# Optimization experiments

Measured on AMD Instinct MI355X. Metric: run time of the kernel, lower is better.

Reference implementation:

```python
import jax, jax.numpy as jnp
import numpy as np

N_NODES = 5000
K_POOL = 30
BN_EPS = 1e-5


def setup_inputs() -> dict:
    key = jax.random.key(0)
    ks = jax.random.split(key, 16)
    B, N, Din, C, H, OUT, E = 32, N_NODES, 16, 64, 128, 2, 80000
    F_tot = Din + 3 * C  # concat of input + 3 conv layers = 208
    return {
        "x": jax.random.normal(ks[0], (B, N, Din), jnp.float32),
        "age": jax.random.uniform(ks[1], (B,), jnp.float32) * 100.0,
        "edge_attr": jax.random.uniform(ks[2], (E,), jnp.float32) + 0.1,
        "W0": jax.random.normal(ks[3], (Din, C), jnp.float32) * 0.1,
        "b0": jnp.zeros((C,), jnp.float32),
        "W1": jax.random.normal(ks[4], (C, C), jnp.float32) * 0.1,
        "b1": jnp.zeros((C,), jnp.float32),
        "W2": jax.random.normal(ks[5], (C, C), jnp.float32) * 0.1,
        "b2": jnp.zeros((C,), jnp.float32),
        "g0": jnp.ones((C,), jnp.float32),
        "be0": jnp.zeros((C,), jnp.float32),
        "g1": jnp.ones((C,), jnp.float32),
        "be1": jnp.zeros((C,), jnp.float32),
        "mW0": jax.random.normal(ks[6], (K_POOL * F_tot + 1, H), jnp.float32) * 0.02,
        "mb0": jnp.zeros((H,), jnp.float32),
        "mW1": jax.random.normal(ks[7], (H, OUT), jnp.float32) * 0.1,
        "mb1": jnp.zeros((OUT,), jnp.float32),
        "edge_row": jax.random.randint(ks[8], (E,), 0, N, jnp.int32),
        "edge_col": jax.random.randint(ks[9], (E,), 0, N, jnp.int32),
    }


def _spmm(xw, rows, cols, nv):
    # xw: (B, N, C); out[b, r] = sum_{edges (r,c)} nv * xw[b, c]
    def one(xb):
        return jax.ops.segment_sum(xb[cols] * nv[:, None], rows, num_segments=N_NODES)
    return jax.vmap(one)(xw)


def reference(x, age, edge_attr, W0, b0, W1, b1, W2, b2, g0, be0, g1, be1,
              mW0, mb0, mW1, mb1, edge_row, edge_col):
    N = N_NODES
    # GCN normalization on A + I (gcn_norm with edge weights, self-loop value 1)
    loop = jnp.arange(N, dtype=edge_row.dtype)
    rows = jnp.concatenate([edge_row, loop])
    cols = jnp.concatenate([edge_col, loop])
    vals = jnp.concatenate([edge_attr, jnp.ones((N,), edge_attr.dtype)])
    deg = jax.ops.segment_sum(vals, rows, num_segments=N)
    dinv = jnp.where(deg > 0, jax.lax.rsqrt(jnp.maximum(deg, 1e-12)), 0.0)
    nv = dinv[rows] * vals * dinv[cols]

    feats = [x]
    h = x
    convs = [(W0, b0), (W1, b1), (W2, b2)]
    bns = [(g0, be0), (g1, be1)]
    for i, (W, b) in enumerate(convs):
        h = _spmm(h @ W, rows, cols, nv) + b  # GCNConv
        if i < len(convs) - 1:
            g, be = bns[i]
            mu = jnp.mean(h, axis=(0, 1))   # BatchNorm1d over flattened (B*N, C)
            var = jnp.var(h, axis=(0, 1))
            h = (h - mu) * jax.lax.rsqrt(var + BN_EPS) * g + be
        h = jax.nn.relu(h)  # dropout p=0.0 -> identity
        feats.append(h)

    z = jnp.concatenate(feats, axis=-1)  # (B, N, 208)
    # global_sort_pool: sort nodes by last feature channel, descending, take top-k
    order = jnp.argsort(-z[:, :, -1], axis=1)[:, :K_POOL]  # (B, k)
    zk = jnp.take_along_axis(z, order[:, :, None], axis=1)  # (B, k, 208)
    flat = zk.reshape(z.shape[0], -1)
    flat = jnp.concatenate([flat, age[:, None]], axis=1)  # append age scalar

    hm = jax.nn.relu(flat @ mW0 + mb0)  # MLP head
    out = hm @ mW1 + mb1
    return jax.nn.log_softmax(out, axis=-1)
```

## Files before the change

### kernel.cpp

```cpp
#include <hip/hip_runtime.h>
#include <math.h>

#define NN    5000
#define NE    80000
#define NB    32
#define DIN   16
#define CH    64
#define KPOOL 30
#define FTOT  208
#define FLATW 6241
#define NH    128
#define NG    8
#define GB    4
#define NPB   16
#define NPAD  5008
#define NEPAD (NE + 4 * NN)
#define NSLOT 32



__global__ void k_init(float* deg, int* counts, float* stats, float* hm, int* perm) {
    int i = blockIdx.x * 256 + threadIdx.x;
    if (i < NN) { deg[i] = 1.0f; counts[i] = 0; }
    if (i < 2 * NSLOT * 128) stats[i] = 0.0f;
    if (i < 4096) hm[i] = 0.0f;
    if (i >= NN && i < NPAD) perm[i] = NN;
}

#define NEB 313
__global__ void k_edgetr(const float* __restrict__ attr, const int* __restrict__ erow,
                         float* deg, int* counts,
                         const float* __restrict__ x, float* __restrict__ xt) {
    if (blockIdx.x < NEB) {
        int e = blockIdx.x * 256 + threadIdx.x;
        if (e < NE) {
            int r = erow[e];
            atomicAdd(&deg[r], attr[e]);
            atomicAdd(&counts[r], 1);
        }
    } else {
        int idx = (blockIdx.x - NEB) * 256 + threadIdx.x;
        if (idx >= NB * NN) return;
        int b = idx / NN, n = idx % NN;
        int g = b >> 2, bi = b & 3;
        const float4* src = (const float4*)(x + (size_t)idx * DIN);
        float4* dst = (float4*)(xt + (((size_t)g * NN + n) * GB + bi) * DIN);
        dst[0] = src[0]; dst[1] = src[1]; dst[2] = src[2]; dst[3] = src[3];
    }
}

__global__ __launch_bounds__(1024) void k_scan(const int* __restrict__ counts,
                                               const float* __restrict__ deg,
                                               int* rowptr, int* cursor, float* dinv,
                                               int* perm) {
    __shared__ int wsum[16], woff[16];
    __shared__ int carry_sh;
    __shared__ int hist[256];
    int t = threadIdx.x;
    int lane = t & 63, wid = t >> 6;
    if (t == 0) carry_sh = 0;
    if (t < 256) hist[t] = 0;
    __syncthreads();
    for (int base = 0; base < NN; base += 1024) {
        int carry = carry_sh;
        int i = base + t;
        int v = 0;
        if (i < NN) {
            v = (counts[i] + 3) & ~3;
            dinv[i] = 1.0f / sqrtf(deg[i]);
            atomicAdd(&hist[255 - min(v >> 2, 255)], 1);
        }
        int s = v;
#pragma unroll
        for (int off = 1; off < 64; off <<= 1) {
            int o = __shfl_up(s, off);
            if (lane >= off) s += o;
        }
        if (lane == 63) wsum[wid] = s;
        __syncthreads();
        if (t < 16) {
            int w = wsum[t];
#pragma unroll
            for (int off = 1; off < 16; off <<= 1) {
                int o = __shfl_up(w, off);
                if (t >= off) w += o;
            }
            woff[t] = w;
        }
        __syncthreads();
        int inc = s + (wid > 0 ? woff[wid - 1] : 0) + carry;
        if (i < NN) {
            rowptr[i + 1] = inc;
            cursor[i] = inc - v;
        }
        if (t == 1023) carry_sh = carry + woff[15];
        __syncthreads();
    }
    if (t == 0) rowptr[0] = 0;
    int mycnt = (t < 256) ? hist[t] : 0;
    for (int off = 1; off < 256; off <<= 1) {
        int v = (t < 256 && t >= off) ? hist[t - off] : 0;
        __syncthreads();
        if (t < 256) hist[t] += v;
        __syncthreads();
    }
    if (t < 256) hist[t] -= mycnt;
    __syncthreads();
    for (int i = t; i < NN; i += 1024) {
        int b = 255 - min(((counts[i] + 3) & ~3) >> 2, 255);
        int pos = atomicAdd(&hist[b], 1);
        perm[pos] = i;
    }
}

__global__ void k_build(const int* __restrict__ erow, const int* __restrict__ ecol,
                        const float* __restrict__ attr, const float* __restrict__ dinv,
                        const int* __restrict__ counts, const int* __restrict__ rowptr,
                        int* cursor, int* csr_col, float* csr_nv) {
    int t = blockIdx.x * 256 + threadIdx.x;
    if (t < NE) {
        int r = erow[t], c = ecol[t];
        int pos = atomicAdd(&cursor[r], 1);
        csr_col[pos] = c;
        csr_nv[pos] = dinv[r] * attr[t] * dinv[c];
    } else if (t - NE < NN) {
        int i = t - NE;
        int cnt = counts[i];
        int pcnt = (cnt + 3) & ~3;
        int base = rowptr[i + 1] - pcnt;
        for (int p = base + cnt; p < base + pcnt; ++p) { csr_col[p] = i; csr_nv[p] = 0.0f; }
    }
}

template<int ACT>
__device__ __forceinline__ float4 actv(float4 v, float4 s, float4 t) {
    if (ACT) {
        v.x = fmaxf(fmaf(v.x, s.x, t.x), 0.f);
        v.y = fmaxf(fmaf(v.y, s.y, t.y), 0.f);
        v.z = fmaxf(fmaf(v.z, s.z, t.z), 0.f);
        v.w = fmaxf(fmaf(v.w, s.w, t.w), 0.f);
    }
    return v;
}
__device__ __forceinline__ void fma4(float4& a, float w, float4 v) {
    a.x = fmaf(w, v.x, a.x); a.y = fmaf(w, v.y, a.y);
    a.z = fmaf(w, v.z, a.z); a.w = fmaf(w, v.w, a.w);
}

template<int CIN, int ACT, int STATS, int SCORE>
__global__ __launch_bounds__(256) void k_layer(
        const float* __restrict__ in, const float* __restrict__ bnstats,
        const float* __restrict__ gamma, const float* __restrict__ beta,
        const float* __restrict__ W, const float* __restrict__ bias,
        const int* __restrict__ rowptr, const int* __restrict__ csr_col,
        const float* __restrict__ csr_nv, const float* __restrict__ dinv,
        const int* __restrict__ perm,
        float* __restrict__ out, float* __restrict__ stats,
        float* __restrict__ score) {
    constexpr int ALS = (CIN == 64) ? 68 : 20;
    __shared__ float As[4 * 16 * ALS];
    __shared__ float stl[ACT ? 128 : 4];
    int tid = threadIdx.x;
    int wid = tid >> 6, lane = tid & 63;
    int g = blockIdx.x & 7;
    int nb = (blockIdx.x >> 3) * NPB;
    int base = nb + wid * 4;
    float* Aw = As + wid * 16 * ALS;
    const int4 pid = *(const int4*)(perm + base);

    if (ACT) {
        if (tid < 64) {
            float su = 0.f, qu = 0.f;
#pragma unroll
            for (int s = 0; s < NSLOT; ++s) {
                su += bnstats[s * 128 + tid];
                qu += bnstats[s * 128 + 64 + tid];
            }
            const float inv = 1.0f / (float)(NB * NN);
            float mu = su * inv;
            float var = qu * inv - mu * mu;
            float sc = gamma[tid] / sqrtf(var + 1e-5f);
            stl[tid] = sc;
            stl[64 + tid] = fmaf(-mu, sc, beta[tid]);
        }
        __syncthreads();
    }

    if (CIN == 64) {
        const float4* __restrict__ in4 = (const float4*)in + (size_t)g * NN * 64;
        int c4 = lane & 15, bi = lane >> 4;
        float4 sv = {1.f,1.f,1.f,1.f}, tv = {0.f,0.f,0.f,0.f};
        if (ACT) { sv = ((const float4*)stl)[c4]; tv = ((const float4*)(stl + 64))[c4]; }
#pragma unroll
        for (int pr = 0; pr < 2; ++pr) {
            int id0 = (pr == 0) ? pid.x : pid.z;
            int id1 = (pr == 0) ? pid.y : pid.w;
            bool vn0 = id0 < NN, vn1 = id1 < NN;
            int rc0 = vn0 ? id0 : 0, rc1 = vn1 ? id1 : 0;
            float dd0 = dinv[rc0]; dd0 *= dd0;
            float dd1 = dinv[rc1]; dd1 *= dd1;
            float4 a0 = {0.f,0.f,0.f,0.f}, a1 = {0.f,0.f,0.f,0.f};
            {
                float4 v0 = actv<ACT>(in4[(size_t)rc0 * 64 + lane], sv, tv);
                float4 v1 = actv<ACT>(in4[(size_t)rc1 * 64 + lane], sv, tv);
                if (vn0) { a0.x = dd0 * v0.x; a0.y = dd0 * v0.y; a0.z = dd0 * v0.z; a0.w = dd0 * v0.w; }
                if (vn1) { a1.x = dd1 * v1.x; a1.y = dd1 * v1.y; a1.z = dd1 * v1.z; a1.w = dd1 * v1.w; }
            }
            int p0a = rowptr[rc0], na = vn0 ? (rowptr[rc0 + 1] - p0a) >> 2 : 0;
            int p0b = rowptr[rc1], nbv = vn1 ? (rowptr[rc1 + 1] - p0b) >> 2 : 0;
            int mx = max(na, nbv);
            for (int bb = 0; bb < mx; ++bb) {
                int ea = min(p0a + 4 * bb, NEPAD - 4);
                int eb = min(p0b + 4 * bb, NEPAD - 4);
                bool va = bb < na, vb = bb < nbv;
                int4   ca = *(const int4*)(csr_col + ea);
                float4 wa = *(const float4*)(csr_nv + ea);
                int4   cb = *(const int4*)(csr_col + eb);
                float4 wb = *(const float4*)(csr_nv + eb);
                if (!va) { wa.x = 0.f; wa.y = 0.f; wa.z = 0.f; wa.w = 0.f;
                           ca.x = 0; ca.y = 0; ca.z = 0; ca.w = 0; }
                if (!vb) { wb.x = 0.f; wb.y = 0.f; wb.z = 0.f; wb.w = 0.f;
                           cb.x = 0; cb.y = 0; cb.z = 0; cb.w = 0; }
                float4 u0 = in4[(size_t)ca.x * 64 + lane];
                float4 u1 = in4[(size_t)ca.y * 64 + lane];
                float4 u2 = in4[(size_t)ca.z * 64 + lane];
                float4 u3 = in4[(size_t)ca.w * 64 + lane];
                float4 t0 = in4[(size_t)cb.x * 64 + lane];
                float4 t1 = in4[(size_t)cb.y * 64 + lane];
                float4 t2 = in4[(size_t)cb.z * 64 + lane];
                float4 t3 = in4[(size_t)cb.w * 64 + lane];
                fma4(a0, wa.x, actv<ACT>(u0, sv, tv));
                fma4(a0, wa.y, actv<ACT>(u1, sv, tv));
                fma4(a0, wa.z, actv<ACT>(u2, sv, tv));
                fma4(a0, wa.w, actv<ACT>(u3, sv, tv));
                fma4(a1, wb.x, actv<ACT>(t0, sv, tv));
                fma4(a1, wb.y, actv<ACT>(t1, sv, tv));
                fma4(a1, wb.z, actv<ACT>(t2, sv, tv));
                fma4(a1, wb.w, actv<ACT>(t3, sv, tv));
            }
            *(float4*)(Aw + ((pr * 2 + 0) * 4 + bi) * ALS + c4 * 4) = a0;
            *(float4*)(Aw + ((pr * 2 + 1) * 4 + bi) * ALS + c4 * 4) = a1;
        }
    } else {
        const float* __restrict__ inr = in + (size_t)g * NN * 64;
        int ids[4] = {pid.x, pid.y, pid.z, pid.w};
#pragma unroll
        for (int i = 0; i < 4; ++i) {
            int r = ids[i];
            float a = 0.f;
            if (r < NN) {
                float d = dinv[r];
                a = d * d * inr[(size_t)r * 64 + lane];
                int p0 = rowptr[r], p1 = rowptr[r + 1];
                for (int e = p0; e < p1; e += 4) {
                    int4   cc = *(const int4*)(csr_col + e);
                    float4 ww = *(const float4*)(csr_nv + e);
                    float v0 = inr[(size_t)cc.x * 64 + lane];
                    float v1 = inr[(size_t)cc.y * 64 + lane];
                    float v2 = inr[(size_t)cc.z * 64 + lane];
                    float v3 = inr[(size_t)cc.w * 64 + lane];
                    a = fmaf(ww.x, v0, a);
                    a = fmaf(ww.y, v1, a);
                    a = fmaf(ww.z, v2, a);
                    a = fmaf(ww.w, v3, a);
                }
            }
            Aw[(i * 4 + (lane >> 4)) * ALS + (lane & 15)] = a;
        }
    }

    int colq = lane & 15, rowq = lane >> 4;
    int node = (rowq == 0) ? pid.x : (rowq == 1) ? pid.y : (rowq == 2) ? pid.z : pid.w;

    if (!SCORE) {
        const float4* __restrict__ W4 = (const float4*)W;
        float4 bb = ((const float4*)bias)[colq];
        float4 o[4];
#pragma unroll
        for (int i = 0; i < 4; ++i) o[i] = bb;
#pragma unroll 8
        for (int k = 0; k < CIN; ++k) {
            float4 w4 = W4[k * 16 + colq];
#pragma unroll
            for (int i = 0; i < 4; ++i) {
                float a = Aw[(rowq * 4 + i) * ALS + k];
                fma4(o[i], a, w4);
            }
        }
        if (node < NN) {
            float4* __restrict__ op = (float4*)(out + ((size_t)g * NN + node) * 256);
#pragma unroll
            for (int i = 0; i < 4; ++i) op[i * 16 + colq] = o[i];
        }

        if (STATS) {
            float4 s4 = {0,0,0,0}, q4 = {0,0,0,0};
            if (node < NN) {
#pragma unroll
                for (int i = 0; i < 4; ++i) {
                    s4.x += o[i].x; s4.y += o[i].y; s4.z += o[i].z; s4.w += o[i].w;
                    q4.x = fmaf(o[i].x, o[i].x, q4.x); q4.y = fmaf(o[i].y, o[i].y, q4.y);
                    q4.z = fmaf(o[i].z, o[i].z, q4.z); q4.w = fmaf(o[i].w, o[i].w, q4.w);
                }
            }
            s4.x += __shfl_xor(s4.x, 16); s4.y += __shfl_xor(s4.y, 16);
            s4.z += __shfl_xor(s4.z, 16); s4.w += __shfl_xor(s4.w, 16);
            q4.x += __shfl_xor(q4.x, 16); q4.y += __shfl_xor(q4.y, 16);
            q4.z += __shfl_xor(q4.z, 16); q4.w += __shfl_xor(q4.w, 16);
            s4.x += __shfl_xor(s4.x, 32); s4.y += __shfl_xor(s4.y, 32);
            s4.z += __shfl_xor(s4.z, 32); s4.w += __shfl_xor(s4.w, 32);
            q4.x += __shfl_xor(q4.x, 32); q4.y += __shfl_xor(q4.y, 32);
            q4.z += __shfl_xor(q4.z, 32); q4.w += __shfl_xor(q4.w, 32);
            __syncthreads();
            if (lane < 16) {
                float* S = As + wid * 128;
                *(float4*)(S + lane * 8) = s4;
                *(float4*)(S + lane * 8 + 4) = q4;
            }
            __syncthreads();
            if (tid < 64) {
                int cq = tid >> 2, comp = tid & 3;
                float s = 0.f, q = 0.f;
#pragma unroll
                for (int w = 0; w < 4; ++w) {
                    s += As[w * 128 + cq * 8 + comp];
                    q += As[w * 128 + cq * 8 + 4 + comp];
                }
                float* sl = stats + (blockIdx.x & (NSLOT - 1)) * 128;
                atomicAdd(&sl[tid], s);
                atomicAdd(&sl[64 + tid], q);
            }
        }
    } else {
        if (node < NN) {
            float4* __restrict__ op = (float4*)(out + ((size_t)g * NN + node) * 256);
#pragma unroll
            for (int i = 0; i < 4; ++i)
                op[i * 16 + colq] = *(const float4*)(Aw + (rowq * 4 + i) * ALS + colq * 4);
        }
        if (lane < 16) {
            int q = lane >> 2;
            int nd = (q == 0) ? pid.x : (q == 1) ? pid.y : (q == 2) ? pid.z : pid.w;
            if (nd < NN) {
                float s = bias[63];
                const float* Ar = Aw + lane * ALS;
#pragma unroll 8
                for (int k = 0; k < 64; ++k)
                    s = fmaf(Ar[k], W[k * 64 + 63], s);
                score[((size_t)g * NN + nd) * 4 + (lane & 3)] = fmaxf(s, 0.f);
            }
        }
    }
}

__global__ void k_bnfin(const float* __restrict__ stats,
                        const float* __restrict__ g0, const float* __restrict__ be0,
                        const float* __restrict__ g1, const float* __restrict__ be1,
                        float* st) {
    int tid = threadIdx.x;
    int c = tid & 63, layer = tid >> 6;
    const float* sb = stats + layer * NSLOT * 128;
    float su = 0.f, qu = 0.f;
#pragma unroll
    for (int s = 0; s < NSLOT; ++s) {
        su += sb[s * 128 + c];
        qu += sb[s * 128 + 64 + c];
    }
    const float inv = 1.0f / (float)(NB * NN);
    float mu = su * inv;
    float var = qu * inv - mu * mu;
    float g = layer ? g1[c] : g0[c];
    float be = layer ? be1[c] : be0[c];
    float sc = g / sqrtf(var + 1e-5f);
    st[layer * 128 + c] = sc;
    st[layer * 128 + 64 + c] = fmaf(-mu, sc, be);
}

__global__ __launch_bounds__(1024) void k_toppool(const float* __restrict__ sc, int* order) {
    __shared__ unsigned long long wbest[16];
    __shared__ unsigned long long winner;
    int b = blockIdx.x, tid = threadIdx.x;
    int g = b >> 2, bi = b & 3;
    int lane = tid & 63, wid = tid >> 6;
    unsigned long long key[5];
#pragma unroll
    for (int j = 0; j < 5; ++j) {
        int n = tid + j * 1024;
        unsigned long long k = 0;
        if (n < NN) {
            float v = sc[((size_t)g * NN + n) * GB + bi];
            k = ((unsigned long long)__float_as_uint(v) << 32) | (unsigned int)(NN - n);
        }
        key[j] = k;
    }
    for (int k = 0; k < KPOOL; ++k) {
        unsigned long long best = key[0];
#pragma unroll
        for (int j = 1; j < 5; ++j) best = (key[j] > best) ? key[j] : best;
#pragma unroll
        for (int off = 1; off < 64; off <<= 1) {
            unsigned long long o = __shfl_xor(best, off);
            best = (o > best) ? o : best;
        }
        if (lane == 0) wbest[wid] = best;
        __syncthreads();
        if (tid == 0) {
            unsigned long long w = wbest[0];
#pragma unroll
            for (int i = 1; i < 16; ++i) w = (wbest[i] > w) ? wbest[i] : w;
            winner = w;
            order[b * KPOOL + k] = NN - (int)(w & 0xFFFFFFFFu);
        }
        __syncthreads();
        int n = NN - (int)(winner & 0xFFFFFFFFu);
        if ((n & 1023) == tid) key[n >> 10] = 0;
    }
}

__global__ void k_gather(const float* __restrict__ xt, const float* __restrict__ h1,
                         const float* __restrict__ h2, const float* __restrict__ agg,
                         const float* __restrict__ W2, const float* __restrict__ b2,
                         const float* __restrict__ st, const float* __restrict__ age,
                         const int* __restrict__ order, float* __restrict__ flat) {
    int bk = blockIdx.x;
    int b = bk / KPOOL, k = bk % KPOOL;
    int n = order[bk];
    int g = b >> 2, bi = b & 3;
    size_t node = (size_t)g * NN + n;
    int f = threadIdx.x;
    float val = 0.f;
    if (f < DIN) {
        val = xt[(node * GB + bi) * DIN + f];
    } else if (f < DIN + CH) {
        int c = f - DIN;
        val = fmaxf(fmaf(h1[(node * GB + bi) * CH + c], st[c], st[64 + c]), 0.f);
    } else if (f < DIN + 2 * CH) {
        int c = f - DIN - CH;
        val = fmaxf(fmaf(h2[(node * GB + bi) * CH + c], st[128 + c], st[192 + c]), 0.f);
    } else if (f < FTOT) {
        int c = f - DIN - 2 * CH;
        const float* __restrict__ Ar = agg + (node * GB + bi) * CH;
        float s = b2[c];
#pragma unroll 8
        for (int kk = 0; kk < 64; ++kk)
            s = fmaf(Ar[kk], W2[kk * 64 + c], s);
        val = fmaxf(s, 0.f);
    }
    if (f < FTOT) flat[(size_t)b * FLATW + k * FTOT + f] = val;
    if (bk == 0 && f >= FTOT && f < FTOT + NB)
        flat[(size_t)(f - FTOT) * FLATW + (FLATW - 1)] = age[f - FTOT];
}

__global__ void k_head1(const float* __restrict__ flat, const float* __restrict__ mW0,
                        float* hm) {
    int tid = threadIdx.x;
    int j4 = (tid & 31) * 4;
    int b0 = (tid >> 5) * 4;
    int kbase = blockIdx.x * 64;
    float acc[4][4];
#pragma unroll
    for (int i = 0; i < 4; i++)
#pragma unroll
        for (int jj = 0; jj < 4; jj++) acc[i][jj] = 0.f;
    int kend = FLATW - kbase; if (kend > 64) kend = 64;
    for (int kk = 0; kk < kend; ++kk) {
        int k = kbase + kk;
        float4 w = *(const float4*)(mW0 + (size_t)k * NH + j4);
#pragma unroll
        for (int i = 0; i < 4; i++) {
            float fv = flat[(size_t)(b0 + i) * FLATW + k];
            acc[i][0] = fmaf(fv, w.x, acc[i][0]);
            acc[i][1] = fmaf(fv, w.y, acc[i][1]);
            acc[i][2] = fmaf(fv, w.z, acc[i][2]);
            acc[i][3] = fmaf(fv, w.w, acc[i][3]);
        }
    }
#pragma unroll
    for (int i = 0; i < 4; i++)
#pragma unroll
        for (int jj = 0; jj < 4; jj++)
            atomicAdd(&hm[(size_t)(b0 + i) * NH + j4 + jj], acc[i][jj]);
}

__global__ void k_head2(const float* __restrict__ hm, const float* __restrict__ mb0,
                        const float* __restrict__ mW1, const float* __restrict__ mb1,
                        float* __restrict__ out) {
    __shared__ float vals[64];
    int tid = threadIdx.x;
    int b = tid >> 1, o = tid & 1;
    float acc = mb1[o];
    for (int j = 0; j < NH; ++j) {
        float hv = fmaxf(hm[b * NH + j] + mb0[j], 0.f);
        acc = fmaf(hv, mW1[j * 2 + o], acc);
    }
    vals[tid] = acc;
    __syncthreads();
    float v0 = vals[b * 2], v1 = vals[b * 2 + 1];
    float m = fmaxf(v0, v1);
    float lse = m + logf(expf(v0 - m) + expf(v1 - m));
    out[tid] = acc - lse;
}

extern "C" void kernel_launch(void* const* d_in, const int* in_sizes, int n_in,
                              void* d_out, int out_size, void* d_ws, size_t ws_size,
                              hipStream_t stream) {
    const float* x    = (const float*)d_in[0];
    const float* age  = (const float*)d_in[1];
    const float* attr = (const float*)d_in[2];
    const float* W0   = (const float*)d_in[3];
    const float* b0   = (const float*)d_in[4];
    const float* W1   = (const float*)d_in[5];
    const float* b1   = (const float*)d_in[6];
    const float* W2   = (const float*)d_in[7];
    const float* b2   = (const float*)d_in[8];
    const float* g0   = (const float*)d_in[9];
    const float* be0  = (const float*)d_in[10];
    const float* g1   = (const float*)d_in[11];
    const float* be1  = (const float*)d_in[12];
    const float* mW0  = (const float*)d_in[13];
    const float* mb0  = (const float*)d_in[14];
    const float* mW1  = (const float*)d_in[15];
    const float* mb1  = (const float*)d_in[16];
    const int* erow   = (const int*)d_in[17];
    const int* ecol   = (const int*)d_in[18];
    float* out = (float*)d_out;

    float* ws     = (float*)d_ws;
    float* deg    = ws;
    float* dinv   = deg + 5008;
    int*   counts = (int*)(dinv + 5008);
    int*   rowptr = counts + 5008;
    int*   cursor = rowptr + 5008;
    int*   perm   = cursor + 5008;
    int*   csr_col= perm + 5008;
    float* csr_nv = (float*)(csr_col + NEPAD);
    float* stats  = csr_nv + NEPAD;
    float* st     = stats + 2 * NSLOT * 128;
    float* sc     = st + 256;
    int*   order  = (int*)(sc + NB * NN);
    float* flat   = (float*)(order + 960);
    float* hm     = flat + (size_t)NB * FLATW;
    float* xt     = hm + 4096;
    float* h1     = xt + (size_t)NB * NN * DIN;
    float* h2     = h1 + (size_t)NB * NN * CH;
    float* agg    = h2 + (size_t)NB * NN * CH;

    k_init<<<32, 256, 0, stream>>>(deg, counts, stats, hm, perm);
    k_edgetr<<<NEB + (NB * NN + 255) / 256, 256, 0, stream>>>(attr, erow, deg, counts, x, xt);
    k_scan<<<1, 1024, 0, stream>>>(counts, deg, rowptr, cursor, dinv, perm);
    k_build<<<(NE + NN + 255) / 256, 256, 0, stream>>>(erow, ecol, attr, dinv, counts, rowptr, cursor, csr_col, csr_nv);

    const int NBLK = ((NN + NPB - 1) / NPB) * NG;
    k_layer<16, 0, 1, 0><<<NBLK, 256, 0, stream>>>(xt, nullptr, nullptr, nullptr, W0, b0, rowptr, csr_col, csr_nv, dinv, perm, h1, stats, nullptr);
    k_layer<64, 1, 1, 0><<<NBLK, 256, 0, stream>>>(h1, stats, g0, be0, W1, b1, rowptr, csr_col, csr_nv, dinv, perm, h2, stats + NSLOT * 128, nullptr);
    k_layer<64, 1, 0, 1><<<NBLK, 256, 0, stream>>>(h2, stats + NSLOT * 128, g1, be1, W2, b2, rowptr, csr_col, csr_nv, dinv, perm, agg, nullptr, sc);

    k_bnfin<<<1, 128, 0, stream>>>(stats, g0, be0, g1, be1, st);
    k_toppool<<<NB, 1024, 0, stream>>>(sc, order);
    k_gather<<<NB * KPOOL, 256, 0, stream>>>(xt, h1, h2, agg, W2, b2, st, age, order, flat);
    k_head1<<<(FLATW + 63) / 64, 256, 0, stream>>>(flat, mW0, hm);
    k_head2<<<1, 64, 0, stream>>>(hm, mb0, mW1, mb1, out);
}
```

Measured before the change: 354.6 us.

## Process five nodes per wave so node chunks tile exactly and drop padding checks

Each wave now handles 5 nodes instead of 4, making 20 nodes per block so 250 chunks cover all 5000 nodes exactly. This removes the padded perm entries and the per-node validity branches. The fifth node's edge loop is split across two accumulators for more memory parallelism. The shared-memory tile drops its row padding in favour of an XOR swizzle, BN scale/shift is computed per lane in registers instead of through shared memory with a barrier, and the launch bounds now ask for higher occupancy. The risks are more register pressure and a fifth, serial edge walk per wave that may raise tail latency on high-degree nodes.

```diff
diff --git a/kernel.cpp b/kernel.cpp
--- a/kernel.cpp
+++ b/kernel.cpp
@@ -12,19 +12,18 @@
 #define NH    128
 #define NG    8
 #define GB    4
-#define NPB   16
-#define NPAD  5008
+#define NPB   20
+#define NCHUNK 250
 #define NEPAD (NE + 4 * NN)
 #define NSLOT 32
 
 
 
-__global__ void k_init(float* deg, int* counts, float* stats, float* hm, int* perm) {
+__global__ void k_init(float* deg, int* counts, float* stats, float* hm) {
     int i = blockIdx.x * 256 + threadIdx.x;
     if (i < NN) { deg[i] = 1.0f; counts[i] = 0; }
     if (i < 2 * NSLOT * 128) stats[i] = 0.0f;
     if (i < 4096) hm[i] = 0.0f;
-    if (i >= NN && i < NPAD) perm[i] = NN;
 }
 
 #define NEB 313
@@ -148,7 +147,7 @@
 }
 
 template<int CIN, int ACT, int STATS, int SCORE>
-__global__ __launch_bounds__(256) void k_layer(
+__global__ __launch_bounds__(256, 8) void k_layer(
         const float* __restrict__ in, const float* __restrict__ bnstats,
         const float* __restrict__ gamma, const float* __restrict__ beta,
         const float* __restrict__ W, const float* __restrict__ bias,
@@ -157,62 +156,60 @@
         const int* __restrict__ perm,
         float* __restrict__ out, float* __restrict__ stats,
         float* __restrict__ score) {
-    constexpr int ALS = (CIN == 64) ? 68 : 20;
-    __shared__ float As[4 * 16 * ALS];
-    __shared__ float stl[ACT ? 128 : 4];
+    constexpr int ALS = (CIN == 64) ? 64 : 20;
+    __shared__ float As[4 * 20 * ALS];
     int tid = threadIdx.x;
     int wid = tid >> 6, lane = tid & 63;
     int g = blockIdx.x & 7;
-    int nb = (blockIdx.x >> 3) * NPB;
-    int base = nb + wid * 4;
-    float* Aw = As + wid * 16 * ALS;
-    const int4 pid = *(const int4*)(perm + base);
-
-    if (ACT) {
-        if (tid < 64) {
-            float su = 0.f, qu = 0.f;
-#pragma unroll
-            for (int s = 0; s < NSLOT; ++s) {
-                su += bnstats[s * 128 + tid];
-                qu += bnstats[s * 128 + 64 + tid];
-            }
-            const float inv = 1.0f / (float)(NB * NN);
-            float mu = su * inv;
-            float var = qu * inv - mu * mu;
-            float sc = gamma[tid] / sqrtf(var + 1e-5f);
-            stl[tid] = sc;
-            stl[64 + tid] = fmaf(-mu, sc, beta[tid]);
-        }
-        __syncthreads();
-    }
+    int base = (blockIdx.x >> 3) * NPB + wid * 5;
+    float* Aw = As + wid * 20 * ALS;
+    int ids[5];
+#pragma unroll
+    for (int j = 0; j < 5; ++j) ids[j] = perm[base + j];
+
+    int c4 = lane & 15, bi = lane >> 4;
 
     if (CIN == 64) {
         const float4* __restrict__ in4 = (const float4*)in + (size_t)g * NN * 64;
-        int c4 = lane & 15, bi = lane >> 4;
         float4 sv = {1.f,1.f,1.f,1.f}, tv = {0.f,0.f,0.f,0.f};
-        if (ACT) { sv = ((const float4*)stl)[c4]; tv = ((const float4*)(stl + 64))[c4]; }
+        if (ACT) {
+            float4 su = {0,0,0,0}, qu = {0,0,0,0};
+#pragma unroll
+            for (int s = 0; s < NSLOT; ++s) {
+                float4 aa = *(const float4*)(bnstats + s * 128 + c4 * 4);
+                float4 bb = *(const float4*)(bnstats + s * 128 + 64 + c4 * 4);
+                su.x += aa.x; su.y += aa.y; su.z += aa.z; su.w += aa.w;
+                qu.x += bb.x; qu.y += bb.y; qu.z += bb.z; qu.w += bb.w;
+            }
+            const float inv = 1.0f / (float)(NB * NN);
+            float4 ga = ((const float4*)gamma)[c4];
+            float4 bt = ((const float4*)beta)[c4];
+            float m, v2;
+            m = su.x * inv; v2 = qu.x * inv - m * m; sv.x = ga.x / sqrtf(v2 + 1e-5f); tv.x = fmaf(-m, sv.x, bt.x);
+            m = su.y * inv; v2 = qu.y * inv - m * m; sv.y = ga.y / sqrtf(v2 + 1e-5f); tv.y = fmaf(-m, sv.y, bt.y);
+            m = su.z * inv; v2 = qu.z * inv - m * m; sv.z = ga.z / sqrtf(v2 + 1e-5f); tv.z = fmaf(-m, sv.z, bt.z);
+            m = su.w * inv; v2 = qu.w * inv - m * m; sv.w = ga.w / sqrtf(v2 + 1e-5f); tv.w = fmaf(-m, sv.w, bt.w);
+        }
+        const int swz = (c4 ^ (bi << 2)) << 2;
 #pragma unroll
         for (int pr = 0; pr < 2; ++pr) {
-            int id0 = (pr == 0) ? pid.x : pid.z;
-            int id1 = (pr == 0) ? pid.y : pid.w;
-            bool vn0 = id0 < NN, vn1 = id1 < NN;
-            int rc0 = vn0 ? id0 : 0, rc1 = vn1 ? id1 : 0;
-            float dd0 = dinv[rc0]; dd0 *= dd0;
-            float dd1 = dinv[rc1]; dd1 *= dd1;
-            float4 a0 = {0.f,0.f,0.f,0.f}, a1 = {0.f,0.f,0.f,0.f};
+            int id0 = ids[2 * pr], id1 = ids[2 * pr + 1];
+            float dd0 = dinv[id0]; dd0 *= dd0;
+            float dd1 = dinv[id1]; dd1 *= dd1;
+            float4 a0, a1;
             {
-                float4 v0 = actv<ACT>(in4[(size_t)rc0 * 64 + lane], sv, tv);
-                float4 v1 = actv<ACT>(in4[(size_t)rc1 * 64 + lane], sv, tv);
-                if (vn0) { a0.x = dd0 * v0.x; a0.y = dd0 * v0.y; a0.z = dd0 * v0.z; a0.w = dd0 * v0.w; }
-                if (vn1) { a1.x = dd1 * v1.x; a1.y = dd1 * v1.y; a1.z = dd1 * v1.z; a1.w = dd1 * v1.w; }
-            }
-            int p0a = rowptr[rc0], na = vn0 ? (rowptr[rc0 + 1] - p0a) >> 2 : 0;
-            int p0b = rowptr[rc1], nbv = vn1 ? (rowptr[rc1 + 1] - p0b) >> 2 : 0;
-            int mx = max(na, nbv);
+                float4 v0 = actv<ACT>(in4[(size_t)id0 * 64 + lane], sv, tv);
+                float4 v1 = actv<ACT>(in4[(size_t)id1 * 64 + lane], sv, tv);
+                a0.x = dd0 * v0.x; a0.y = dd0 * v0.y; a0.z = dd0 * v0.z; a0.w = dd0 * v0.w;
+                a1.x = dd1 * v1.x; a1.y = dd1 * v1.y; a1.z = dd1 * v1.z; a1.w = dd1 * v1.w;
+            }
+            int p0a = rowptr[id0], na = (rowptr[id0 + 1] - p0a) >> 2;
+            int p0b = rowptr[id1], nb2 = (rowptr[id1 + 1] - p0b) >> 2;
+            int mx = max(na, nb2);
             for (int bb = 0; bb < mx; ++bb) {
                 int ea = min(p0a + 4 * bb, NEPAD - 4);
                 int eb = min(p0b + 4 * bb, NEPAD - 4);
-                bool va = bb < na, vb = bb < nbv;
+                bool va = bb < na, vb = bb < nb2;
                 int4   ca = *(const int4*)(csr_col + ea);
                 float4 wa = *(const float4*)(csr_nv + ea);
                 int4   cb = *(const int4*)(csr_col + eb);
@@ -238,70 +235,101 @@
                 fma4(a1, wb.z, actv<ACT>(t2, sv, tv));
                 fma4(a1, wb.w, actv<ACT>(t3, sv, tv));
             }
-            *(float4*)(Aw + ((pr * 2 + 0) * 4 + bi) * ALS + c4 * 4) = a0;
-            *(float4*)(Aw + ((pr * 2 + 1) * 4 + bi) * ALS + c4 * 4) = a1;
+            *(float4*)(Aw + ((2 * pr + 0) * 4 + bi) * 64 + swz) = a0;
+            *(float4*)(Aw + ((2 * pr + 1) * 4 + bi) * 64 + swz) = a1;
+        }
+        {
+            int r = ids[4];
+            float dd = dinv[r]; dd *= dd;
+            float4 v = actv<ACT>(in4[(size_t)r * 64 + lane], sv, tv);
+            float4 a0 = {dd * v.x, dd * v.y, dd * v.z, dd * v.w};
+            float4 a1 = {0.f, 0.f, 0.f, 0.f};
+            int p0 = rowptr[r];
+            int n4 = (rowptr[r + 1] - p0) >> 2;
+            int na = (n4 + 1) >> 1, nb2 = n4 >> 1;
+            for (int bb = 0; bb < na; ++bb) {
+                int ea = p0 + 8 * bb;
+                int eb = min(ea + 4, NEPAD - 4);
+                bool vb = bb < nb2;
+                int4   ca = *(const int4*)(csr_col + ea);
+                float4 wa = *(const float4*)(csr_nv + ea);
+                int4   cb = *(const int4*)(csr_col + eb);
+                float4 wb = *(const float4*)(csr_nv + eb);
+                if (!vb) { wb.x = 0.f; wb.y = 0.f; wb.z = 0.f; wb.w = 0.f;
+                           cb.x = 0; cb.y = 0; cb.z = 0; cb.w = 0; }
+                float4 u0 = in4[(size_t)ca.x * 64 + lane];
+                float4 u1 = in4[(size_t)ca.y * 64 + lane];
+                float4 u2 = in4[(size_t)ca.z * 64 + lane];
+                float4 u3 = in4[(size_t)ca.w * 64 + lane];
+                float4 t0 = in4[(size_t)cb.x * 64 + lane];
+                float4 t1 = in4[(size_t)cb.y * 64 + lane];
+                float4 t2 = in4[(size_t)cb.z * 64 + lane];
+                float4 t3 = in4[(size_t)cb.w * 64 + lane];
+                fma4(a0, wa.x, actv<ACT>(u0, sv, tv));
+                fma4(a0, wa.y, actv<ACT>(u1, sv, tv));
+                fma4(a0, wa.z, actv<ACT>(u2, sv, tv));
+                fma4(a0, wa.w, actv<ACT>(u3, sv, tv));
+                fma4(a1, wb.x, actv<ACT>(t0, sv, tv));
+                fma4(a1, wb.y, actv<ACT>(t1, sv, tv));
+                fma4(a1, wb.z, actv<ACT>(t2, sv, tv));
+                fma4(a1, wb.w, actv<ACT>(t3, sv, tv));
+            }
+            a0.x += a1.x; a0.y += a1.y; a0.z += a1.z; a0.w += a1.w;
+            *(float4*)(Aw + (16 + bi) * 64 + swz) = a0;
         }
     } else {
         const float* __restrict__ inr = in + (size_t)g * NN * 64;
-        int ids[4] = {pid.x, pid.y, pid.z, pid.w};
-#pragma unroll
-        for (int i = 0; i < 4; ++i) {
+#pragma unroll
+        for (int i = 0; i < 5; ++i) {
             int r = ids[i];
-            float a = 0.f;
-            if (r < NN) {
-                float d = dinv[r];
-                a = d * d * inr[(size_t)r * 64 + lane];
-                int p0 = rowptr[r], p1 = rowptr[r + 1];
-                for (int e = p0; e < p1; e += 4) {
-                    int4   cc = *(const int4*)(csr_col + e);
-                    float4 ww = *(const float4*)(csr_nv + e);
-                    float v0 = inr[(size_t)cc.x * 64 + lane];
-                    float v1 = inr[(size_t)cc.y * 64 + lane];
-                    float v2 = inr[(size_t)cc.z * 64 + lane];
-                    float v3 = inr[(size_t)cc.w * 64 + lane];
-                    a = fmaf(ww.x, v0, a);
-                    a = fmaf(ww.y, v1, a);
-                    a = fmaf(ww.z, v2, a);
-                    a = fmaf(ww.w, v3, a);
-                }
-            }
-            Aw[(i * 4 + (lane >> 4)) * ALS + (lane & 15)] = a;
-        }
-    }
-
-    int colq = lane & 15, rowq = lane >> 4;
-    int node = (rowq == 0) ? pid.x : (rowq == 1) ? pid.y : (rowq == 2) ? pid.z : pid.w;
+            float d = dinv[r];
+            float a = d * d * inr[(size_t)r * 64 + lane];
+            int p0 = rowptr[r], p1 = rowptr[r + 1];
+            for (int e = p0; e < p1; e += 4) {
+                int4   cc = *(const int4*)(csr_col + e);
+                float4 ww = *(const float4*)(csr_nv + e);
+                float v0 = inr[(size_t)cc.x * 64 + lane];
+                float v1 = inr[(size_t)cc.y * 64 + lane];
+                float v2 = inr[(size_t)cc.z * 64 + lane];
+                float v3 = inr[(size_t)cc.w * 64 + lane];
+                a = fmaf(ww.x, v0, a);
+                a = fmaf(ww.y, v1, a);
+                a = fmaf(ww.z, v2, a);
+                a = fmaf(ww.w, v3, a);
+            }
+            Aw[(i * 4 + bi) * ALS + c4] = a;
+        }
+    }
 
     if (!SCORE) {
         const float4* __restrict__ W4 = (const float4*)W;
-        float4 bb = ((const float4*)bias)[colq];
-        float4 o[4];
-#pragma unroll
-        for (int i = 0; i < 4; ++i) o[i] = bb;
+        float4 bb4 = ((const float4*)bias)[c4];
+        float4 o[5];
+#pragma unroll
+        for (int i = 0; i < 5; ++i) o[i] = bb4;
 #pragma unroll 8
         for (int k = 0; k < CIN; ++k) {
-            float4 w4 = W4[k * 16 + colq];
-#pragma unroll
-            for (int i = 0; i < 4; ++i) {
-                float a = Aw[(rowq * 4 + i) * ALS + k];
+            float4 w4 = W4[k * 16 + c4];
+            int krd = (CIN == 64) ? (k ^ (bi << 4)) : k;
+#pragma unroll
+            for (int i = 0; i < 5; ++i) {
+                float a = Aw[(i * 4 + bi) * ALS + krd];
                 fma4(o[i], a, w4);
             }
         }
-        if (node < NN) {
-            float4* __restrict__ op = (float4*)(out + ((size_t)g * NN + node) * 256);
-#pragma unroll
-            for (int i = 0; i < 4; ++i) op[i * 16 + colq] = o[i];
+#pragma unroll
+        for (int i = 0; i < 5; ++i) {
+            float4* __restrict__ op = (float4*)(out + ((size_t)g * NN + ids[i]) * 256);
+            op[bi * 16 + c4] = o[i];
         }
 
         if (STATS) {
             float4 s4 = {0,0,0,0}, q4 = {0,0,0,0};
-            if (node < NN) {
-#pragma unroll
-                for (int i = 0; i < 4; ++i) {
-                    s4.x += o[i].x; s4.y += o[i].y; s4.z += o[i].z; s4.w += o[i].w;
-                    q4.x = fmaf(o[i].x, o[i].x, q4.x); q4.y = fmaf(o[i].y, o[i].y, q4.y);
-                    q4.z = fmaf(o[i].z, o[i].z, q4.z); q4.w = fmaf(o[i].w, o[i].w, q4.w);
-                }
+#pragma unroll
+            for (int i = 0; i < 5; ++i) {
+                s4.x += o[i].x; s4.y += o[i].y; s4.z += o[i].z; s4.w += o[i].w;
+                q4.x = fmaf(o[i].x, o[i].x, q4.x); q4.y = fmaf(o[i].y, o[i].y, q4.y);
+                q4.z = fmaf(o[i].z, o[i].z, q4.z); q4.w = fmaf(o[i].w, o[i].w, q4.w);
             }
             s4.x += __shfl_xor(s4.x, 16); s4.y += __shfl_xor(s4.y, 16);
             s4.z += __shfl_xor(s4.z, 16); s4.w += __shfl_xor(s4.w, 16);
@@ -332,23 +360,21 @@
             }
         }
     } else {
-        if (node < NN) {
-            float4* __restrict__ op = (float4*)(out + ((size_t)g * NN + node) * 256);
-#pragma unroll
-            for (int i = 0; i < 4; ++i)
-                op[i * 16 + colq] = *(const float4*)(Aw + (rowq * 4 + i) * ALS + colq * 4);
-        }
-        if (lane < 16) {
+#pragma unroll
+        for (int i = 0; i < 5; ++i) {
+            float4* __restrict__ op = (float4*)(out + ((size_t)g * NN + ids[i]) * 256);
+            op[bi * 16 + c4] = *(const float4*)(Aw + (i * 4 + bi) * 64 + ((c4 ^ (bi << 2)) << 2));
+        }
+        if (lane < 20) {
             int q = lane >> 2;
-            int nd = (q == 0) ? pid.x : (q == 1) ? pid.y : (q == 2) ? pid.z : pid.w;
-            if (nd < NN) {
-                float s = bias[63];
-                const float* Ar = Aw + lane * ALS;
+            int nd = (q == 0) ? ids[0] : (q == 1) ? ids[1] : (q == 2) ? ids[2]
+                   : (q == 3) ? ids[3] : ids[4];
+            float s = bias[63];
+            int sw = (lane & 3) << 4;
 #pragma unroll 8
-                for (int k = 0; k < 64; ++k)
-                    s = fmaf(Ar[k], W[k * 64 + 63], s);
-                score[((size_t)g * NN + nd) * 4 + (lane & 3)] = fmaxf(s, 0.f);
-            }
+            for (int k = 0; k < 64; ++k)
+                s = fmaf(Aw[lane * 64 + (k ^ sw)], W[k * 64 + 63], s);
+            score[((size_t)g * NN + nd) * 4 + (lane & 3)] = fmaxf(s, 0.f);
         }
     }
 }
@@ -545,12 +571,12 @@
     float* h2     = h1 + (size_t)NB * NN * CH;
     float* agg    = h2 + (size_t)NB * NN * CH;
 
-    k_init<<<32, 256, 0, stream>>>(deg, counts, stats, hm, perm);
+    k_init<<<32, 256, 0, stream>>>(deg, counts, stats, hm);
     k_edgetr<<<NEB + (NB * NN + 255) / 256, 256, 0, stream>>>(attr, erow, deg, counts, x, xt);
     k_scan<<<1, 1024, 0, stream>>>(counts, deg, rowptr, cursor, dinv, perm);
     k_build<<<(NE + NN + 255) / 256, 256, 0, stream>>>(erow, ecol, attr, dinv, counts, rowptr, cursor, csr_col, csr_nv);
 
-    const int NBLK = ((NN + NPB - 1) / NPB) * NG;
+    const int NBLK = NCHUNK * NG;
     k_layer<16, 0, 1, 0><<<NBLK, 256, 0, stream>>>(xt, nullptr, nullptr, nullptr, W0, b0, rowptr, csr_col, csr_nv, dinv, perm, h1, stats, nullptr);
     k_layer<64, 1, 1, 0><<<NBLK, 256, 0, stream>>>(h1, stats, g0, be0, W1, b1, rowptr, csr_col, csr_nv, dinv, perm, h2, stats + NSLOT * 128, nullptr);
     k_layer<64, 1, 0, 1><<<NBLK, 256, 0, stream>>>(h2, stats + NSLOT * 128, g1, be1, W2, b2, rowptr, csr_col, csr_nv, dinv, perm, agg, nullptr, sc);
```

Result: slower. 460.5 us (+29.9%).

## Restructure graph setup kernels and fold BN finalize into top-k pool launch

Applied to the files above, without the earlier changes.

Splits the edge-degree pass from the x transpose, and moves the transpose into a new phase1 kernel. That kernel runs the rowptr scan and the degree-bucket histogram/perm in two separate blocks, which run concurrently rather than serially inside one block. The BN-stat finalize becomes an extra block of the top-k pool kernel, which removes a launch. The MLP head's final kernel splits its 128-long dot products across 4 threads each, and CSR build uses 1024-thread blocks. The changes aim to cut serial single-block time and launch count, at the cost of a more complex kernel structure.

```diff
diff --git a/kernel.cpp b/kernel.cpp
--- a/kernel.cpp
+++ b/kernel.cpp
@@ -13,6 +13,7 @@
 #define NG    8
 #define GB    4
 #define NPB   16
+#define NCHUNK 313
 #define NPAD  5008
 #define NEPAD (NE + 4 * NN)
 #define NSLOT 32
@@ -28,96 +29,104 @@
 }
 
 #define NEB 313
-__global__ void k_edgetr(const float* __restrict__ attr, const int* __restrict__ erow,
-                         float* deg, int* counts,
-                         const float* __restrict__ x, float* __restrict__ xt) {
-    if (blockIdx.x < NEB) {
-        int e = blockIdx.x * 256 + threadIdx.x;
-        if (e < NE) {
-            int r = erow[e];
-            atomicAdd(&deg[r], attr[e]);
-            atomicAdd(&counts[r], 1);
-        }
-    } else {
-        int idx = (blockIdx.x - NEB) * 256 + threadIdx.x;
+__global__ void k_edges(const float* __restrict__ attr, const int* __restrict__ erow,
+                        float* deg, int* counts) {
+    int e = blockIdx.x * 256 + threadIdx.x;
+    if (e < NE) {
+        int r = erow[e];
+        atomicAdd(&deg[r], attr[e]);
+        atomicAdd(&counts[r], 1);
+    }
+}
+
+__global__ __launch_bounds__(1024) void k_phase1(
+        const int* __restrict__ counts, const float* __restrict__ deg,
+        int* rowptr, int* cursor, float* dinv, int* perm,
+        const float* __restrict__ x, float* __restrict__ xt) {
+    __shared__ int wsum[16], woff[16];
+    __shared__ int carry_sh;
+    __shared__ int hist[256];
+    int t = threadIdx.x;
+    if (blockIdx.x >= 2) {
+        int idx = (blockIdx.x - 2) * 1024 + t;
         if (idx >= NB * NN) return;
         int b = idx / NN, n = idx % NN;
         int g = b >> 2, bi = b & 3;
         const float4* src = (const float4*)(x + (size_t)idx * DIN);
         float4* dst = (float4*)(xt + (((size_t)g * NN + n) * GB + bi) * DIN);
         dst[0] = src[0]; dst[1] = src[1]; dst[2] = src[2]; dst[3] = src[3];
-    }
-}
-
-__global__ __launch_bounds__(1024) void k_scan(const int* __restrict__ counts,
-                                               const float* __restrict__ deg,
-                                               int* rowptr, int* cursor, float* dinv,
-                                               int* perm) {
-    __shared__ int wsum[16], woff[16];
-    __shared__ int carry_sh;
-    __shared__ int hist[256];
-    int t = threadIdx.x;
-    int lane = t & 63, wid = t >> 6;
-    if (t == 0) carry_sh = 0;
-    if (t < 256) hist[t] = 0;
-    __syncthreads();
-    for (int base = 0; base < NN; base += 1024) {
-        int carry = carry_sh;
-        int i = base + t;
-        int v = 0;
-        if (i < NN) {
-            v = (counts[i] + 3) & ~3;
-            dinv[i] = 1.0f / sqrtf(deg[i]);
-            atomicAdd(&hist[255 - min(v >> 2, 255)], 1);
-        }
-        int s = v;
-#pragma unroll
-        for (int off = 1; off < 64; off <<= 1) {
-            int o = __shfl_up(s, off);
-            if (lane >= off) s += o;
-        }
-        if (lane == 63) wsum[wid] = s;
-        __syncthreads();
-        if (t < 16) {
-            int w = wsum[t];
-#pragma unroll
-            for (int off = 1; off < 16; off <<= 1) {
-                int o = __shfl_up(w, off);
-                if (t >= off) w += o;
-            }
-            woff[t] = w;
-        }
-        __syncthreads();
-        int inc = s + (wid > 0 ? woff[wid - 1] : 0) + carry;
-        if (i < NN) {
-            rowptr[i + 1] = inc;
-            cursor[i] = inc - v;
-        }
-        if (t == 1023) carry_sh = carry + woff[15];
-        __syncthreads();
-    }
-    if (t == 0) rowptr[0] = 0;
-    int mycnt = (t < 256) ? hist[t] : 0;
-    for (int off = 1; off < 256; off <<= 1) {
-        int v = (t < 256 && t >= off) ? hist[t - off] : 0;
-        __syncthreads();
-        if (t < 256) hist[t] += v;
-        __syncthreads();
-    }
-    if (t < 256) hist[t] -= mycnt;
-    __syncthreads();
-    for (int i = t; i < NN; i += 1024) {
-        int b = 255 - min(((counts[i] + 3) & ~3) >> 2, 255);
-        int pos = atomicAdd(&hist[b], 1);
-        perm[pos] = i;
-    }
-}
-
-__global__ void k_build(const int* __restrict__ erow, const int* __restrict__ ecol,
-                        const float* __restrict__ attr, const float* __restrict__ dinv,
-                        const int* __restrict__ counts, const int* __restrict__ rowptr,
-                        int* cursor, int* csr_col, float* csr_nv) {
-    int t = blockIdx.x * 256 + threadIdx.x;
+        return;
+    }
+    if (blockIdx.x == 0) {
+        int lane = t & 63, wid = t >> 6;
+        if (t == 0) carry_sh = 0;
+        __syncthreads();
+        for (int base = 0; base < NN; base += 1024) {
+            int carry = carry_sh;
+            int i = base + t;
+            int v = 0;
+            if (i < NN) {
+                v = (counts[i] + 3) & ~3;
+                dinv[i] = 1.0f / sqrtf(deg[i]);
+            }
+            int s = v;
+#pragma unroll
+            for (int off = 1; off < 64; off <<= 1) {
+                int o = __shfl_up(s, off);
+                if (lane >= off) s += o;
+            }
+            if (lane == 63) wsum[wid] = s;
+            __syncthreads();
+            if (t < 16) {
+                int w = wsum[t];
+#pragma unroll
+                for (int off = 1; off < 16; off <<= 1) {
+                    int o = __shfl_up(w, off);
+                    if (t >= off) w += o;
+                }
+                woff[t] = w;
+            }
+            __syncthreads();
+            int inc = s + (wid > 0 ? woff[wid - 1] : 0) + carry;
+            if (i < NN) {
+                rowptr[i + 1] = inc;
+                cursor[i] = inc - v;
+            }
+            if (t == 1023) carry_sh = carry + woff[15];
+            __syncthreads();
+        }
+        if (t == 0) rowptr[0] = 0;
+    } else {
+        if (t < 256) hist[t] = 0;
+        __syncthreads();
+        for (int i = t; i < NN; i += 1024) {
+            int b = 255 - min(((counts[i] + 3) & ~3) >> 2, 255);
+            atomicAdd(&hist[b], 1);
+        }
+        __syncthreads();
+        int mycnt = (t < 256) ? hist[t] : 0;
+        for (int off = 1; off < 256; off <<= 1) {
+            int v = (t < 256 && t >= off) ? hist[t - off] : 0;
+            __syncthreads();
+            if (t < 256) hist[t] += v;
+            __syncthreads();
+        }
+        if (t < 256) hist[t] -= mycnt;
+        __syncthreads();
+        for (int i = t; i < NN; i += 1024) {
+            int b = 255 - min(((counts[i] + 3) & ~3) >> 2, 255);
+            int pos = atomicAdd(&hist[b], 1);
+            perm[pos] = i;
+        }
+    }
+}
+
+__global__ __launch_bounds__(1024) void k_build(
+        const int* __restrict__ erow, const int* __restrict__ ecol,
+        const float* __restrict__ attr, const float* __restrict__ dinv,
+        const int* __restrict__ counts, const int* __restrict__ rowptr,
+        int* cursor, int* csr_col, float* csr_nv) {
+    int t = blockIdx.x * 1024 + threadIdx.x;
     if (t < NE) {
         int r = erow[t], c = ecol[t];
         int pos = atomicAdd(&cursor[r], 1);
@@ -310,7 +319,7 @@
             s4.x += __shfl_xor(s4.x, 32); s4.y += __shfl_xor(s4.y, 32);
             s4.z += __shfl_xor(s4.z, 32); s4.w += __shfl_xor(s4.w, 32);
             q4.x += __shfl_xor(q4.x, 32); q4.y += __shfl_xor(q4.y, 32);
-            q4.z += __shfl_xor(q4.z, 32); q4.w += __shfl_xor(q4.w, 32);
+            q4.w += __shfl_xor(q4.w, 32); q4.z += __shfl_xor(q4.z, 32);
             __syncthreads();
             if (lane < 16) {
                 float* S = As + wid * 128;
@@ -353,33 +362,36 @@
     }
 }
 
-__global__ void k_bnfin(const float* __restrict__ stats,
-                        const float* __restrict__ g0, const float* __restrict__ be0,
-                        const float* __restrict__ g1, const float* __restrict__ be1,
-                        float* st) {
-    int tid = threadIdx.x;
-    int c = tid & 63, layer = tid >> 6;
-    const float* sb = stats + layer * NSLOT * 128;
-    float su = 0.f, qu = 0.f;
-#pragma unroll
-    for (int s = 0; s < NSLOT; ++s) {
-        su += sb[s * 128 + c];
-        qu += sb[s * 128 + 64 + c];
-    }
-    const float inv = 1.0f / (float)(NB * NN);
-    float mu = su * inv;
-    float var = qu * inv - mu * mu;
-    float g = layer ? g1[c] : g0[c];
-    float be = layer ? be1[c] : be0[c];
-    float sc = g / sqrtf(var + 1e-5f);
-    st[layer * 128 + c] = sc;
-    st[layer * 128 + 64 + c] = fmaf(-mu, sc, be);
-}
-
-__global__ __launch_bounds__(1024) void k_toppool(const float* __restrict__ sc, int* order) {
+__global__ __launch_bounds__(1024) void k_toppool(const float* __restrict__ sc, int* order,
+        const float* __restrict__ stats,
+        const float* __restrict__ g0, const float* __restrict__ be0,
+        const float* __restrict__ g1, const float* __restrict__ be1,
+        float* __restrict__ st) {
     __shared__ unsigned long long wbest[16];
     __shared__ unsigned long long winner;
-    int b = blockIdx.x, tid = threadIdx.x;
+    int tid = threadIdx.x;
+    if (blockIdx.x == NB) {
+        if (tid < 128) {
+            int c = tid & 63, layer = tid >> 6;
+            const float* sb = stats + layer * NSLOT * 128;
+            float su = 0.f, qu = 0.f;
+#pragma unroll
+            for (int s = 0; s < NSLOT; ++s) {
+                su += sb[s * 128 + c];
+                qu += sb[s * 128 + 64 + c];
+            }
+            const float inv = 1.0f / (float)(NB * NN);
+            float mu = su * inv;
+            float var = qu * inv - mu * mu;
+            float g = layer ? g1[c] : g0[c];
+            float be = layer ? be1[c] : be0[c];
+            float scv = g / sqrtf(var + 1e-5f);
+            st[layer * 128 + c] = scv;
+            st[layer * 128 + 64 + c] = fmaf(-mu, scv, be);
+        }
+        return;
+    }
+    int b = blockIdx.x;
     int g = b >> 2, bi = b & 3;
     int lane = tid & 63, wid = tid >> 6;
     unsigned long long key[5];
@@ -485,20 +497,30 @@
 __global__ void k_head2(const float* __restrict__ hm, const float* __restrict__ mb0,
                         const float* __restrict__ mW1, const float* __restrict__ mb1,
                         float* __restrict__ out) {
+    __shared__ float part[256];
     __shared__ float vals[64];
     int tid = threadIdx.x;
-    int b = tid >> 1, o = tid & 1;
-    float acc = mb1[o];
-    for (int j = 0; j < NH; ++j) {
+    int q = tid & 3, o = (tid >> 2) & 1, b = tid >> 3;
+    float acc = 0.f;
+    for (int j = q * 32; j < q * 32 + 32; ++j) {
         float hv = fmaxf(hm[b * NH + j] + mb0[j], 0.f);
         acc = fmaf(hv, mW1[j * 2 + o], acc);
     }
-    vals[tid] = acc;
+    part[tid] = acc;
     __syncthreads();
-    float v0 = vals[b * 2], v1 = vals[b * 2 + 1];
-    float m = fmaxf(v0, v1);
-    float lse = m + logf(expf(v0 - m) + expf(v1 - m));
-    out[tid] = acc - lse;
+    if (tid < 64) {
+        int b2 = tid >> 1, o2 = tid & 1;
+        int base = (b2 << 3) + (o2 << 2);
+        vals[tid] = part[base] + part[base + 1] + part[base + 2] + part[base + 3] + mb1[o2];
+    }
+    __syncthreads();
+    if (tid < 64) {
+        int b2 = tid >> 1;
+        float v0 = vals[b2 * 2], v1 = vals[b2 * 2 + 1];
+        float m = fmaxf(v0, v1);
+        float lse = m + logf(expf(v0 - m) + expf(v1 - m));
+        out[tid] = vals[tid] - lse;
+    }
 }
 
 extern "C" void kernel_launch(void* const* d_in, const int* in_sizes, int n_in,
@@ -546,18 +568,17 @@
     float* agg    = h2 + (size_t)NB * NN * CH;
 
     k_init<<<32, 256, 0, stream>>>(deg, counts, stats, hm, perm);
-    k_edgetr<<<NEB + (NB * NN + 255) / 256, 256, 0, stream>>>(attr, erow, deg, counts, x, xt);
-    k_scan<<<1, 1024, 0, stream>>>(counts, deg, rowptr, cursor, dinv, perm);
-    k_build<<<(NE + NN + 255) / 256, 256, 0, stream>>>(erow, ecol, attr, dinv, counts, rowptr, cursor, csr_col, csr_nv);
-
-    const int NBLK = ((NN + NPB - 1) / NPB) * NG;
+    k_edges<<<NEB, 256, 0, stream>>>(attr, erow, deg, counts);
+    k_phase1<<<2 + (NB * NN + 1023) / 1024, 1024, 0, stream>>>(counts, deg, rowptr, cursor, dinv, perm, x, xt);
+    k_build<<<(NE + NN + 1023) / 1024, 1024, 0, stream>>>(erow, ecol, attr, dinv, counts, rowptr, cursor, csr_col, csr_nv);
+
+    const int NBLK = NCHUNK * NG;
     k_layer<16, 0, 1, 0><<<NBLK, 256, 0, stream>>>(xt, nullptr, nullptr, nullptr, W0, b0, rowptr, csr_col, csr_nv, dinv, perm, h1, stats, nullptr);
     k_layer<64, 1, 1, 0><<<NBLK, 256, 0, stream>>>(h1, stats, g0, be0, W1, b1, rowptr, csr_col, csr_nv, dinv, perm, h2, stats + NSLOT * 128, nullptr);
     k_layer<64, 1, 0, 1><<<NBLK, 256, 0, stream>>>(h2, stats + NSLOT * 128, g1, be1, W2, b2, rowptr, csr_col, csr_nv, dinv, perm, agg, nullptr, sc);
 
-    k_bnfin<<<1, 128, 0, stream>>>(stats, g0, be0, g1, be1, st);
-    k_toppool<<<NB, 1024, 0, stream>>>(sc, order);
+    k_toppool<<<NB + 1, 1024, 0, stream>>>(sc, order, stats, g0, be0, g1, be1, st);
     k_gather<<<NB * KPOOL, 256, 0, stream>>>(xt, h1, h2, agg, W2, b2, st, age, order, flat);
     k_head1<<<(FLATW + 63) / 64, 256, 0, stream>>>(flat, mW0, hm);
-    k_head2<<<1, 64, 0, stream>>>(hm, mb0, mW1, mb1, out);
-}
+    k_head2<<<1, 256, 0, stream>>>(hm, mb0, mW1, mb1, out);
+}
```

Result: no change. 348.6 us (-1.7%).
